# Performance work log

Measured on AMD Instinct MI355X. Metric: run time of the kernel, lower is better.

## Reference

```python
import jax, jax.numpy as jnp
import numpy as np

D = 64        # GatedGraphConv out_channels
N_LAYERS = 5  # number of stacked convs


def setup_inputs() -> dict:
    key = jax.random.key(0)
    ks = jax.random.split(key, 16)
    N, E, G = 100000, 1600000, 64
    s = 0.1
    inp = {
        'conv_weight': jax.random.normal(ks[0], (N_LAYERS, D, D), jnp.float32) * s,
        'gru_w_ih':    jax.random.normal(ks[1], (N_LAYERS, 3 * D, D), jnp.float32) * s,
        'gru_w_hh':    jax.random.normal(ks[2], (N_LAYERS, 3 * D, D), jnp.float32) * s,
        'gru_b_ih':    jax.random.normal(ks[3], (N_LAYERS, 3 * D), jnp.float32) * s,
        'gru_b_hh':    jax.random.normal(ks[4], (N_LAYERS, 3 * D), jnp.float32) * s,
        'fc1_w': jax.random.normal(ks[5], (32, D), jnp.float32) * s,
        'fc1_b': jax.random.normal(ks[6], (32,), jnp.float32) * s,
        'fc2_w': jax.random.normal(ks[7], (16, 32), jnp.float32) * s,
        'fc2_b': jax.random.normal(ks[8], (16,), jnp.float32) * s,
        'fc3_w': jax.random.normal(ks[9], (1, 16), jnp.float32) * s,
        'fc3_b': jax.random.normal(ks[10], (1,), jnp.float32) * s,
        'edge_index': jax.random.randint(ks[11], (2, E), 0, N, jnp.int64 if jax.config.jax_enable_x64 else jnp.int32),
        'batch': jnp.sort(jax.random.randint(ks[12], (N,), 0, G, jnp.int32)),
        'num_nodes': N,
        'num_graphs': G,
    }
    return inp


def _gru_cell(m, h, w_ih, w_hh, b_ih, b_hh):
    # torch.nn.GRUCell math; m: [N,D] input, h: [N,D] hidden
    gi = m @ w_ih.T + b_ih   # [N, 3D]
    gh = h @ w_hh.T + b_hh   # [N, 3D]
    i_r, i_z, i_n = jnp.split(gi, 3, axis=1)
    h_r, h_z, h_n = jnp.split(gh, 3, axis=1)
    r = jax.nn.sigmoid(i_r + h_r)
    z = jax.nn.sigmoid(i_z + h_z)
    n = jnp.tanh(i_n + r * h_n)
    return (1.0 - z) * n + z * h


def reference(conv_weight, gru_w_ih, gru_w_hh, gru_b_ih, gru_b_hh,
              fc1_w, fc1_b, fc2_w, fc2_b, fc3_w, fc3_b,
              edge_index, batch, num_nodes, num_graphs):
    src, dst = edge_index[0], edge_index[1]  # source_to_target flow
    # initial node features: zeros [N,8] zero-padded to D by GatedGraphConv
    x0 = jnp.zeros((num_nodes, D), jnp.float32)

    def step(x, params):
        w, wih, whh, bih, bhh = params
        m = x @ w                                        # [N, D]
        agg = jax.ops.segment_sum(m[src], dst, num_segments=num_nodes)  # scatter-add
        return _gru_cell(agg, x, wih, whh, bih, bhh), None

    x, _ = jax.lax.scan(step, x0,
                        (conv_weight, gru_w_ih, gru_w_hh, gru_b_ih, gru_b_hh))

    # scatter_add pooling over batch -> [num_graphs, D]
    g = jax.ops.segment_sum(x, batch, num_segments=num_graphs)
    h = jax.nn.elu(g @ fc1_w.T + fc1_b)
    h = jax.nn.elu(h @ fc2_w.T + fc2_b)
    return h @ fc3_w.T + fc3_b  # [num_graphs, 1]
```

## Files before the change

### kernel.cpp

```cpp
#include <hip/hip_runtime.h>
#include <math.h>

typedef _Float16 f16x2 __attribute__((ext_vector_type(2)));
typedef _Float16 f16x4 __attribute__((ext_vector_type(4)));
typedef _Float16 f16x8 __attribute__((ext_vector_type(8)));
typedef float f32x4 __attribute__((ext_vector_type(4)));

#define CBITS 10
#define FCHUNK 4096
#define MATSZ 13056
__device__ __forceinline__ int woff(int row) { return 64 * row + 8 * (row >> 1); }

__device__ __forceinline__ float sigmoidf_(float v) {
  return 1.0f / (1.0f + __expf(-v));
}
__device__ __forceinline__ float tanhf_(float v) {
  v = fminf(fmaxf(v, -15.f), 15.f);
  float e = __expf(2.f * v);
  return (e - 1.f) / (e + 1.f);
}
__device__ __forceinline__ float eluf_(float v) { return v > 0.f ? v : (__expf(v) - 1.f); }

__global__ __launch_bounds__(256) void fuse_w_kernel(const float* __restrict__ conv_w,
                                                     const float* __restrict__ w_ih,
                                                     _Float16* __restrict__ wcS) {
  const int l = blockIdx.x >> 2;
  const int j0 = (blockIdx.x & 3) * 48;
  const float* W = conv_w + (size_t)l * 4096;
  const float* wi = w_ih + (size_t)l * 12288;
  _Float16* out = wcS + (size_t)l * MATSZ;
  __shared__ float sWt[64 * 68];
  __shared__ float sI[48 * 64];
  const int t = threadIdx.x;
  for (int i = t; i < 4096; i += 256) sWt[(i & 63) * 68 + (i >> 6)] = W[i];
  for (int i = t; i < 3072; i += 256) sI[i] = wi[j0 * 64 + i];
  __syncthreads();
#pragma unroll
  for (int r = 0; r < 3; ++r) {
    int u = t + 256 * r;
    int j = u >> 4, cg = (u & 15) * 4;
    float4 a = {0.f, 0.f, 0.f, 0.f};
    for (int k = 0; k < 64; ++k) {
      float4 w = *(const float4*)(sWt + k * 68 + cg);
      float s = sI[j * 64 + k];
      a.x += w.x * s; a.y += w.y * s; a.z += w.z * s; a.w += w.w * s;
    }
    int row = j0 + j;
    f16x4 hv;
    hv[0] = (_Float16)a.x; hv[1] = (_Float16)a.y;
    hv[2] = (_Float16)a.z; hv[3] = (_Float16)a.w;
    *(f16x4*)(out + woff(row) + cg) = hv;
  }
}

__global__ __launch_bounds__(256) void whh_prep_kernel(const float* __restrict__ whh,
                                                       _Float16* __restrict__ whhS) {
  int idx = blockIdx.x * 256 + threadIdx.x;
  if (idx >= 15360) return;
  int l = idx / 3072, rem = idx % 3072;
  int r = rem >> 4, c4 = (rem & 15) * 4;
  float4 v = *(const float4*)(whh + (size_t)l * 12288 + r * 64 + c4);
  f16x4 hv;
  hv[0] = (_Float16)v.x; hv[1] = (_Float16)v.y;
  hv[2] = (_Float16)v.z; hv[3] = (_Float16)v.w;
  *(f16x4*)(whhS + (size_t)l * MATSZ + woff(r) + c4) = hv;
}

__global__ __launch_bounds__(256) void bucket_hist_kernel(const int* __restrict__ dst,
                                                          int* __restrict__ bh, int E) {
  __shared__ int h[128];
  const int t = threadIdx.x;
  if (t < 128) h[t] = 0;
  __syncthreads();
  for (int e = blockIdx.x * 256 + t; e < E; e += gridDim.x * 256)
    atomicAdd(&h[dst[e] >> CBITS], 1);
  __syncthreads();
  if (t < 128 && h[t]) atomicAdd(&bh[t * 16], h[t]);
}

__global__ __launch_bounds__(128) void bucket_scan_kernel(int* __restrict__ bh, int nbk,
                                                          int* __restrict__ boffs, int E) {
  __shared__ int s[128];
  const int t = threadIdx.x;
  int v = (t < nbk) ? bh[t * 16] : 0;
  s[t] = v;
  __syncthreads();
  for (int o = 1; o < 128; o <<= 1) {
    int a = (t >= o) ? s[t - o] : 0;
    __syncthreads();
    s[t] += a;
    __syncthreads();
  }
  if (t < nbk) {
    int ex = s[t] - v;
    boffs[t] = ex;
    bh[t * 16] = ex;
  }
  if (t == 0) boffs[nbk] = E;
}

__global__ __launch_bounds__(256) void bucket_fill_kernel(const int* __restrict__ src,
                                                          const int* __restrict__ dst,
                                                          int* __restrict__ bcur,
                                                          unsigned* __restrict__ pairs, int E) {
  __shared__ uint2 staged[FCHUNK];
  __shared__ int h[128], lbase[128], gbase[128], lcur[128];
  const int t = threadIdx.x;
  const int e0 = blockIdx.x * FCHUNK;
  int cnt = E - e0;
  if (cnt > FCHUNK) cnt = FCHUNK;
  if (t < 128) h[t] = 0;
  __syncthreads();
  for (int i = t; i < cnt; i += 256) atomicAdd(&h[dst[e0 + i] >> CBITS], 1);
  __syncthreads();
  if (t < 128) lcur[t] = h[t];
  __syncthreads();
  for (int o = 1; o < 128; o <<= 1) {
    int a = 0;
    if (t < 128 && t >= o) a = lcur[t - o];
    __syncthreads();
    if (t < 128) lcur[t] += a;
    __syncthreads();
  }
  if (t < 128) {
    int ex = lcur[t] - h[t];
    lbase[t] = ex;
    if (h[t]) gbase[t] = atomicAdd(&bcur[t * 16], h[t]);
    lcur[t] = ex;
  }
  __syncthreads();
  for (int i = t; i < cnt; i += 256) {
    int d = dst[e0 + i];
    int b = d >> CBITS;
    int p = atomicAdd(&lcur[b], 1);
    staged[p] = make_uint2((unsigned)src[e0 + i], (unsigned)d);
  }
  __syncthreads();
  for (int i = t; i < cnt; i += 256) {
    uint2 pr = staged[i];
    int b = (int)(pr.y >> CBITS);
    pairs[gbase[b] + (i - lbase[b])] = (pr.x << CBITS) | (pr.y & ((1u << CBITS) - 1));
  }
}

__global__ __launch_bounds__(256) void csr_build_kernel(const unsigned* __restrict__ pairs,
                                                        const int* __restrict__ boffs,
                                                        int* __restrict__ offs,
                                                        int* __restrict__ srcs, int N, int E) {
  const int b = blockIdx.x, t = threadIdx.x;
  const int nbase = b << CBITS;
  __shared__ int deg[1024];
  __shared__ int ssc[256];
  for (int i = t; i < 1024; i += 256) deg[i] = 0;
  __syncthreads();
  const int beg = boffs[b], end = boffs[b + 1];
  for (int e = beg + t; e < end; e += 256) atomicAdd(&deg[pairs[e] & 1023], 1);
  __syncthreads();
  int d0 = deg[4 * t], d1 = deg[4 * t + 1], d2 = deg[4 * t + 2], d3 = deg[4 * t + 3];
  int s = d0 + d1 + d2 + d3;
  ssc[t] = s;
  __syncthreads();
  for (int o = 1; o < 256; o <<= 1) {
    int a = (t >= o) ? ssc[t - o] : 0;
    __syncthreads();
    ssc[t] += a;
    __syncthreads();
  }
  int base = beg + ssc[t] - s;
  int c0 = base, c1 = c0 + d0, c2 = c1 + d1, c3 = c2 + d2;
  if (nbase + 4 * t + 0 < N) offs[nbase + 4 * t + 0] = c0;
  if (nbase + 4 * t + 1 < N) offs[nbase + 4 * t + 1] = c1;
  if (nbase + 4 * t + 2 < N) offs[nbase + 4 * t + 2] = c2;
  if (nbase + 4 * t + 3 < N) offs[nbase + 4 * t + 3] = c3;
  deg[4 * t] = c0; deg[4 * t + 1] = c1; deg[4 * t + 2] = c2; deg[4 * t + 3] = c3;
  if (b == 0 && t == 0) offs[N] = E;
  if (b == 0 && t < 64) srcs[E + t] = 0;
  __syncthreads();
  for (int e = beg + t; e < end; e += 256) {
    unsigned p = pairs[e];
    int pos = atomicAdd(&deg[p & 1023], 1);
    srcs[pos] = (int)(p >> CBITS);
  }
}

__global__ __launch_bounds__(64) void h1_kernel(const float* __restrict__ b_ih,
                                                const float* __restrict__ b_hh,
                                                float* __restrict__ h1) {
  int d = threadIdx.x;
  float r = sigmoidf_(b_ih[d] + b_hh[d]);
  float z = sigmoidf_(b_ih[64 + d] + b_hh[64 + d]);
  float n = tanhf_(b_ih[128 + d] + r * b_hh[128 + d]);
  h1[d] = (1.f - z) * n;
}

__global__ __launch_bounds__(256) void l1u_kernel(const _Float16* __restrict__ wcS1,
                                                  const _Float16* __restrict__ whhS1,
                                                  const float* __restrict__ h1,
                                                  const float* __restrict__ b_ih1,
                                                  const float* __restrict__ b_hh1,
                                                  float* __restrict__ u,
                                                  float* __restrict__ cons) {
  int j = threadIdx.x;
  if (j >= 192) return;
  float su = 0.f, sg = 0.f;
  const int base = woff(j);
  for (int c = 0; c < 64; ++c) {
    float hc = h1[c];
    su += hc * (float)wcS1[base + c];
    sg += hc * (float)whhS1[base + c];
  }
  u[j] = su;
  if (j < 128) {
    cons[j] = sg + b_ih1[j] + b_hh1[j];
  } else {
    cons[j] = b_ih1[j];
    cons[j + 64] = sg + b_hh1[j];
  }
}

__global__ __launch_bounds__(256) void l1_elem_kernel(const int* __restrict__ offs,
                                                      const float* __restrict__ h1,
                                                      const float* __restrict__ u,
                                                      const float* __restrict__ cons,
                                                      _Float16* __restrict__ xh,
                                                      int N, int units) {
  int idx = blockIdx.x * 256 + threadIdx.x;
  if (idx >= units) return;
  int v = idx >> 5, lp = idx & 31;
  float dg = (v < N) ? (float)(offs[v + 1] - offs[v]) : 0.f;
  f16x2 o;
#pragma unroll
  for (int k = 0; k < 2; ++k) {
    int d = 2 * lp + k;
    float r = sigmoidf_(dg * u[d] + cons[d]);
    float z = sigmoidf_(dg * u[64 + d] + cons[64 + d]);
    float n = tanhf_(dg * u[128 + d] + cons[128 + d] + r * cons[192 + d]);
    o[k] = (_Float16)(n + z * (h1[d] - n));
  }
  *(f16x2*)(xh + (size_t)idx * 2) = o;
}

__global__ __launch_bounds__(256) void agg_kernel(const _Float16* __restrict__ xh,
                                                  const int* __restrict__ offs,
                                                  const int* __restrict__ srcs,
                                                  _Float16* __restrict__ aggh, int N) {
  int wave = threadIdx.x >> 6, lane = threadIdx.x & 63;
  int v = blockIdx.x * 4 + wave;
  if (v >= N) return;
  const int beg = offs[v], end = offs[v + 1];
  const int deg = end - beg;
  const int og = lane >> 3;
  const int lp = lane & 7;
  f16x8 acc = {};
  for (int base = 0; base < deg; base += 64) {
    const int cnt = min(64, deg - base);
    int sidx = srcs[beg + base + lane];
    for (int e = 0; e < cnt; e += 8) {
      int me = e + og;
      int s = __shfl(sidx, me);
      f16x8 vv = *(const f16x8*)(xh + (size_t)s * 64 + lp * 8);
      if (me < cnt) acc += vv;
    }
  }
#pragma unroll
  for (int off = 8; off < 64; off <<= 1) {
    union { f16x8 h; int i[4]; } a, b;
    a.h = acc;
#pragma unroll
    for (int w = 0; w < 4; ++w) b.i[w] = __shfl_xor(a.i[w], off);
    acc += b.h;
  }
  if (og == 0) *(f16x8*)(aggh + (size_t)v * 64 + lp * 8) = acc;
}

__global__ __launch_bounds__(256) void gru_kernel(const _Float16* __restrict__ aggh,
                                                  const _Float16* __restrict__ xh_in,
                                                  _Float16* __restrict__ xh_out,
                                                  const _Float16* __restrict__ wcS,
                                                  const _Float16* __restrict__ whhS,
                                                  const float* __restrict__ b_ih,
                                                  const float* __restrict__ b_hh,
                                                  int N, int numIter) {
  __shared__ _Float16 sW[2 * MATSZ];
  const int t = threadIdx.x;
  for (int i = t; i < 2 * (MATSZ / 8); i += 256) {
    int mat = (i >= MATSZ / 8);
    int idx = i - mat * (MATSZ / 8);
    *(f16x8*)(sW + mat * MATSZ + idx * 8) =
        *(const f16x8*)((mat ? whhS : wcS) + idx * 8);
  }
  __syncthreads();
  const int wave = t >> 6, lane = t & 63;
  const int q = lane >> 4, c = lane & 15;
  float bRZ[4], bZZ[4], bIN[4], bHN[4];
#pragma unroll
  for (int dt = 0; dt < 4; ++dt) {
    int d = dt * 16 + c;
    bRZ[dt] = b_ih[d] + b_hh[d];
    bZZ[dt] = b_ih[64 + d] + b_hh[64 + d];
    bIN[dt] = b_ih[128 + d];
    bHN[dt] = b_hh[128 + d];
  }
  f16x8 idf[2];
#pragma unroll
  for (int p = 0; p < 2; ++p) {
    int tgt = p * 16 + c - q * 8;
#pragma unroll
    for (int j = 0; j < 8; ++j) idf[p][j] = (j == tgt) ? (_Float16)1.0f : (_Float16)0.0f;
  }
#pragma unroll 1
  for (int it = blockIdx.x; it < numIter; it += gridDim.x) {
    const int tile = it >> 1, half = it & 1;
    const int nb0 = tile * 64 + wave * 16;
    const size_t rowbase = (size_t)(nb0 + c) * 64;
    f16x8 aA[2], aH[2];
#pragma unroll
    for (int ks = 0; ks < 2; ++ks) {
      aA[ks] = *(const f16x8*)(aggh + rowbase + ks * 32 + q * 8);
      aH[ks] = *(const f16x8*)(xh_in + rowbase + ks * 32 + q * 8);
    }
    f32x4 aR[2], aZ[2], aN[2], aHNa[2], aHO[2];
#pragma unroll
    for (int p = 0; p < 2; ++p) {
      float brz = half ? bRZ[2 + p] : bRZ[p];
      float bzz = half ? bZZ[2 + p] : bZZ[p];
      float bin = half ? bIN[2 + p] : bIN[p];
      float bhn = half ? bHN[2 + p] : bHN[p];
      aR[p] = (f32x4){brz, brz, brz, brz};
      aZ[p] = (f32x4){bzz, bzz, bzz, bzz};
      aN[p] = (f32x4){bin, bin, bin, bin};
      aHNa[p] = (f32x4){bhn, bhn, bhn, bhn};
      aHO[p] = (f32x4){0.f, 0.f, 0.f, 0.f};
    }
#pragma unroll
    for (int ks = 0; ks < 2; ++ks) {
      const int colo = ks * 32 + q * 8;
#pragma unroll
      for (int p = 0; p < 2; ++p) {
        const int r0 = (half * 2 + p) * 16 + c;
        f16x8 bWr = *(const f16x8*)(sW + woff(r0) + colo);
        f16x8 bHr = *(const f16x8*)(sW + MATSZ + woff(r0) + colo);
        f16x8 bWz = *(const f16x8*)(sW + woff(64 + r0) + colo);
        f16x8 bHz = *(const f16x8*)(sW + MATSZ + woff(64 + r0) + colo);
        f16x8 bWn = *(const f16x8*)(sW + woff(128 + r0) + colo);
        f16x8 bHn = *(const f16x8*)(sW + MATSZ + woff(128 + r0) + colo);
        aR[p] = __builtin_amdgcn_mfma_f32_16x16x32_f16(aA[ks], bWr, aR[p], 0, 0, 0);
        aR[p] = __builtin_amdgcn_mfma_f32_16x16x32_f16(aH[ks], bHr, aR[p], 0, 0, 0);
        aZ[p] = __builtin_amdgcn_mfma_f32_16x16x32_f16(aA[ks], bWz, aZ[p], 0, 0, 0);
        aZ[p] = __builtin_amdgcn_mfma_f32_16x16x32_f16(aH[ks], bHz, aZ[p], 0, 0, 0);
        aN[p] = __builtin_amdgcn_mfma_f32_16x16x32_f16(aA[ks], bWn, aN[p], 0, 0, 0);
        aHNa[p] = __builtin_amdgcn_mfma_f32_16x16x32_f16(aH[ks], bHn, aHNa[p], 0, 0, 0);
      }
    }
#pragma unroll
    for (int p = 0; p < 2; ++p)
      aHO[p] = __builtin_amdgcn_mfma_f32_16x16x32_f16(aH[half], idf[p], aHO[p], 0, 0, 0);
#pragma unroll
    for (int p = 0; p < 2; ++p) {
      int d = (half * 2 + p) * 16 + c;
#pragma unroll
      for (int r = 0; r < 4; ++r) {
        int node = nb0 + q * 4 + r;
        if (node < N) {
          float rr = sigmoidf_(aR[p][r]);
          float zz = sigmoidf_(aZ[p][r]);
          float nn = tanhf_(aN[p][r] + rr * aHNa[p][r]);
          float out = nn + zz * (aHO[p][r] - nn);
          xh_out[(size_t)node * 64 + d] = (_Float16)out;
        }
      }
    }
  }
}

__global__ __launch_bounds__(256) void pool_kernel(const _Float16* __restrict__ xh,
                                                   const int* __restrict__ batch,
                                                   float* __restrict__ g, int N) {
  int wave = threadIdx.x >> 6, lane = threadIdx.x & 63;
  int n0 = blockIdx.x * 64 + wave * 16;
  if (n0 >= N) return;
  int end = n0 + 16;
  if (end > N) end = N;
  int cur = batch[n0];
  float acc = 0.f;
  for (int n = n0; n < end; ++n) {
    int b = batch[n];
    if (b != cur) {
      atomicAdd(&g[(size_t)cur * 64 + lane], acc);
      acc = 0.f;
      cur = b;
    }
    acc += (float)xh[(size_t)n * 64 + lane];
  }
  atomicAdd(&g[(size_t)cur * 64 + lane], acc);
}

__global__ __launch_bounds__(256) void mlp_kernel(const float* __restrict__ g,
                                                  const float* __restrict__ w1,
                                                  const float* __restrict__ b1,
                                                  const float* __restrict__ w2,
                                                  const float* __restrict__ b2,
                                                  const float* __restrict__ w3,
                                                  const float* __restrict__ b3,
                                                  float* __restrict__ out, int G) {
  __shared__ float sG[64 * 64];
  __shared__ float sH1[64 * 32];
  __shared__ float sH2[64 * 16];
  int t = threadIdx.x;
  for (int i = t; i < G * 64; i += 256) sG[i] = g[i];
  __syncthreads();
  for (int o = t; o < G * 32; o += 256) {
    int gi = o >> 5, i = o & 31;
    float a = b1[i];
    for (int k = 0; k < 64; ++k) a += sG[gi * 64 + k] * w1[i * 64 + k];
    sH1[gi * 32 + i] = eluf_(a);
  }
  __syncthreads();
  for (int o = t; o < G * 16; o += 256) {
    int gi = o >> 4, i = o & 15;
    float a = b2[i];
    for (int k = 0; k < 32; ++k) a += sH1[gi * 32 + k] * w2[i * 32 + k];
    sH2[gi * 16 + i] = eluf_(a);
  }
  __syncthreads();
  for (int o = t; o < G; o += 256) {
    float a = b3[0];
    for (int k = 0; k < 16; ++k) a += sH2[o * 16 + k] * w3[k];
    out[o] = a;
  }
}

extern "C" void kernel_launch(void* const* d_in, const int* in_sizes, int n_in,
                              void* d_out, int out_size, void* d_ws, size_t ws_size,
                              hipStream_t stream) {
  const float* conv_w = (const float*)d_in[0];
  const float* w_ih = (const float*)d_in[1];
  const float* w_hh = (const float*)d_in[2];
  const float* b_ih = (const float*)d_in[3];
  const float* b_hh = (const float*)d_in[4];
  const float* fc1_w = (const float*)d_in[5];
  const float* fc1_b = (const float*)d_in[6];
  const float* fc2_w = (const float*)d_in[7];
  const float* fc2_b = (const float*)d_in[8];
  const float* fc3_w = (const float*)d_in[9];
  const float* fc3_b = (const float*)d_in[10];
  const int* ei = (const int*)d_in[11];
  const int* batch = (const int*)d_in[12];
  const int N = in_sizes[12];
  const int E = in_sizes[11] / 2;
  const int G = out_size;
  const int* src = ei;
  const int* dst = ei + E;
  const int nbk = (N + 1023) >> CBITS;
  const int tiles = (N + 63) / 64;
  const int Npad = tiles * 64;
  const int gruIter = tiles * 2;

  char* ws = (char*)d_ws;
  size_t off = 0;
  auto alloc = [&](size_t bytes) -> void* {
    void* p = ws + off;
    off += (bytes + 255) & ~(size_t)255;
    return p;
  };
  _Float16* xhA = (_Float16*)alloc((size_t)Npad * 64 * 2);
  _Float16* xhB = (_Float16*)alloc((size_t)Npad * 64 * 2);
  _Float16* aggh = (_Float16*)alloc((size_t)Npad * 64 * 2);
  _Float16* wcS = (_Float16*)alloc((size_t)5 * MATSZ * 2);
  _Float16* whhS = (_Float16*)alloc((size_t)5 * MATSZ * 2);
  float* h1 = (float*)alloc(64 * 4);
  float* l1u = (float*)alloc(192 * 4);
  float* l1c = (float*)alloc(256 * 4);
  float* gbuf = (float*)alloc((size_t)G * 64 * 4);
  int* offs = (int*)alloc((size_t)(N + 1) * 4);
  int* srcs = (int*)alloc((size_t)(E + 64) * 4);
  unsigned* pairs = (unsigned*)alloc((size_t)E * 4);
  int* bh = (int*)alloc(128 * 16 * 4);
  int* boffs = (int*)alloc(129 * 4);

  hipMemsetAsync(bh, 0, 128 * 16 * 4, stream);
  bucket_hist_kernel<<<256, 256, 0, stream>>>(dst, bh, E);
  bucket_scan_kernel<<<1, 128, 0, stream>>>(bh, nbk, boffs, E);
  bucket_fill_kernel<<<(E + FCHUNK - 1) / FCHUNK, 256, 0, stream>>>(src, dst, bh, pairs, E);
  csr_build_kernel<<<nbk, 256, 0, stream>>>(pairs, boffs, offs, srcs, N, E);

  fuse_w_kernel<<<20, 256, 0, stream>>>(conv_w, w_ih, wcS);
  whh_prep_kernel<<<60, 256, 0, stream>>>(w_hh, whhS);

  h1_kernel<<<1, 64, 0, stream>>>(b_ih, b_hh, h1);
  l1u_kernel<<<1, 256, 0, stream>>>(wcS + MATSZ, whhS + MATSZ, h1,
                                    b_ih + 192, b_hh + 192, l1u, l1c);
  l1_elem_kernel<<<(Npad * 32 + 255) / 256, 256, 0, stream>>>(offs, h1, l1u, l1c, xhA,
                                                              N, Npad * 32);

  _Float16* cur = xhA;
  _Float16* nxt = xhB;
  for (int l = 2; l < 5; ++l) {
    agg_kernel<<<(N + 3) / 4, 256, 0, stream>>>(cur, offs, srcs, aggh, N);
    gru_kernel<<<768, 256, 0, stream>>>(aggh, cur, nxt, wcS + (size_t)l * MATSZ,
                                        whhS + (size_t)l * MATSZ, b_ih + (size_t)l * 192,
                                        b_hh + (size_t)l * 192, N, gruIter);
    _Float16* tmp = cur; cur = nxt; nxt = tmp;
  }

  hipMemsetAsync(gbuf, 0, (size_t)G * 64 * 4, stream);
  pool_kernel<<<(N + 63) / 64, 256, 0, stream>>>(cur, batch, gbuf, N);
  mlp_kernel<<<1, 256, 0, stream>>>(gbuf, fc1_w, fc1_b, fc2_w, fc2_b, fc3_w, fc3_b,
                                    (float*)d_out, G);
}
```

Baseline: 409.5 us.

## Drop GRU shared-memory weight staging, merge tiny prep kernels, fold memset

The GRU kernel no longer copies both weight matrices into LDS per block and instead reads B-fragments straight from global memory (through the caches), and it is now launched with gruIter blocks instead of a fixed 768. The h1 and layer-1 prep kernels are merged into one launch, and the pooling buffer memset is folded into the bucket scan kernel. This removes the per-block LDS fill and barrier plus two launches, but the repeated global weight loads inside the MFMA loop depend on L1/L2 hits and could add latency.

```diff
diff --git a/kernel.cpp b/kernel.cpp
--- a/kernel.cpp
+++ b/kernel.cpp
@@ -79,9 +79,11 @@
 }
 
 __global__ __launch_bounds__(128) void bucket_scan_kernel(int* __restrict__ bh, int nbk,
-                                                          int* __restrict__ boffs, int E) {
+                                                          int* __restrict__ boffs, int E,
+                                                          float* __restrict__ gbuf, int gn) {
   __shared__ int s[128];
   const int t = threadIdx.x;
+  for (int i = t; i < gn; i += 128) gbuf[i] = 0.f;
   int v = (t < nbk) ? bh[t * 16] : 0;
   s[t] = v;
   __syncthreads();
@@ -183,29 +185,31 @@
   }
 }
 
-__global__ __launch_bounds__(64) void h1_kernel(const float* __restrict__ b_ih,
-                                                const float* __restrict__ b_hh,
-                                                float* __restrict__ h1) {
-  int d = threadIdx.x;
-  float r = sigmoidf_(b_ih[d] + b_hh[d]);
-  float z = sigmoidf_(b_ih[64 + d] + b_hh[64 + d]);
-  float n = tanhf_(b_ih[128 + d] + r * b_hh[128 + d]);
-  h1[d] = (1.f - z) * n;
-}
-
-__global__ __launch_bounds__(256) void l1u_kernel(const _Float16* __restrict__ wcS1,
-                                                  const _Float16* __restrict__ whhS1,
-                                                  const float* __restrict__ h1,
-                                                  const float* __restrict__ b_ih1,
-                                                  const float* __restrict__ b_hh1,
-                                                  float* __restrict__ u,
-                                                  float* __restrict__ cons) {
+__global__ __launch_bounds__(256) void l01_prep_kernel(const float* __restrict__ b_ih0,
+                                                       const float* __restrict__ b_hh0,
+                                                       const _Float16* __restrict__ wcS1,
+                                                       const _Float16* __restrict__ whhS1,
+                                                       const float* __restrict__ b_ih1,
+                                                       const float* __restrict__ b_hh1,
+                                                       float* __restrict__ h1,
+                                                       float* __restrict__ u,
+                                                       float* __restrict__ cons) {
+  __shared__ float sh1[64];
   int j = threadIdx.x;
+  if (j < 64) {
+    float r = sigmoidf_(b_ih0[j] + b_hh0[j]);
+    float z = sigmoidf_(b_ih0[64 + j] + b_hh0[64 + j]);
+    float n = tanhf_(b_ih0[128 + j] + r * b_hh0[128 + j]);
+    float h = (1.f - z) * n;
+    sh1[j] = h;
+    h1[j] = h;
+  }
+  __syncthreads();
   if (j >= 192) return;
   float su = 0.f, sg = 0.f;
   const int base = woff(j);
   for (int c = 0; c < 64; ++c) {
-    float hc = h1[c];
+    float hc = sh1[c];
     su += hc * (float)wcS1[base + c];
     sg += hc * (float)whhS1[base + c];
   }
@@ -281,15 +285,7 @@
                                                   const float* __restrict__ b_ih,
                                                   const float* __restrict__ b_hh,
                                                   int N, int numIter) {
-  __shared__ _Float16 sW[2 * MATSZ];
   const int t = threadIdx.x;
-  for (int i = t; i < 2 * (MATSZ / 8); i += 256) {
-    int mat = (i >= MATSZ / 8);
-    int idx = i - mat * (MATSZ / 8);
-    *(f16x8*)(sW + mat * MATSZ + idx * 8) =
-        *(const f16x8*)((mat ? whhS : wcS) + idx * 8);
-  }
-  __syncthreads();
   const int wave = t >> 6, lane = t & 63;
   const int q = lane >> 4, c = lane & 15;
   float bRZ[4], bZZ[4], bIN[4], bHN[4];
@@ -338,12 +334,12 @@
 #pragma unroll
       for (int p = 0; p < 2; ++p) {
         const int r0 = (half * 2 + p) * 16 + c;
-        f16x8 bWr = *(const f16x8*)(sW + woff(r0) + colo);
-        f16x8 bHr = *(const f16x8*)(sW + MATSZ + woff(r0) + colo);
-        f16x8 bWz = *(const f16x8*)(sW + woff(64 + r0) + colo);
-        f16x8 bHz = *(const f16x8*)(sW + MATSZ + woff(64 + r0) + colo);
-        f16x8 bWn = *(const f16x8*)(sW + woff(128 + r0) + colo);
-        f16x8 bHn = *(const f16x8*)(sW + MATSZ + woff(128 + r0) + colo);
+        f16x8 bWr = *(const f16x8*)(wcS + woff(r0) + colo);
+        f16x8 bHr = *(const f16x8*)(whhS + woff(r0) + colo);
+        f16x8 bWz = *(const f16x8*)(wcS + woff(64 + r0) + colo);
+        f16x8 bHz = *(const f16x8*)(whhS + woff(64 + r0) + colo);
+        f16x8 bWn = *(const f16x8*)(wcS + woff(128 + r0) + colo);
+        f16x8 bHn = *(const f16x8*)(whhS + woff(128 + r0) + colo);
         aR[p] = __builtin_amdgcn_mfma_f32_16x16x32_f16(aA[ks], bWr, aR[p], 0, 0, 0);
         aR[p] = __builtin_amdgcn_mfma_f32_16x16x32_f16(aH[ks], bHr, aR[p], 0, 0, 0);
         aZ[p] = __builtin_amdgcn_mfma_f32_16x16x32_f16(aA[ks], bWz, aZ[p], 0, 0, 0);
@@ -480,16 +476,15 @@
 
   hipMemsetAsync(bh, 0, 128 * 16 * 4, stream);
   bucket_hist_kernel<<<256, 256, 0, stream>>>(dst, bh, E);
-  bucket_scan_kernel<<<1, 128, 0, stream>>>(bh, nbk, boffs, E);
+  bucket_scan_kernel<<<1, 128, 0, stream>>>(bh, nbk, boffs, E, gbuf, G * 64);
   bucket_fill_kernel<<<(E + FCHUNK - 1) / FCHUNK, 256, 0, stream>>>(src, dst, bh, pairs, E);
   csr_build_kernel<<<nbk, 256, 0, stream>>>(pairs, boffs, offs, srcs, N, E);
 
   fuse_w_kernel<<<20, 256, 0, stream>>>(conv_w, w_ih, wcS);
   whh_prep_kernel<<<60, 256, 0, stream>>>(w_hh, whhS);
 
-  h1_kernel<<<1, 64, 0, stream>>>(b_ih, b_hh, h1);
-  l1u_kernel<<<1, 256, 0, stream>>>(wcS + MATSZ, whhS + MATSZ, h1,
-                                    b_ih + 192, b_hh + 192, l1u, l1c);
+  l01_prep_kernel<<<1, 256, 0, stream>>>(b_ih, b_hh, wcS + MATSZ, whhS + MATSZ,
+                                         b_ih + 192, b_hh + 192, h1, l1u, l1c);
   l1_elem_kernel<<<(Npad * 32 + 255) / 256, 256, 0, stream>>>(offs, h1, l1u, l1c, xhA,
                                                               N, Npad * 32);
 
@@ -497,13 +492,12 @@
   _Float16* nxt = xhB;
   for (int l = 2; l < 5; ++l) {
     agg_kernel<<<(N + 3) / 4, 256, 0, stream>>>(cur, offs, srcs, aggh, N);
-    gru_kernel<<<768, 256, 0, stream>>>(aggh, cur, nxt, wcS + (size_t)l * MATSZ,
-                                        whhS + (size_t)l * MATSZ, b_ih + (size_t)l * 192,
-                                        b_hh + (size_t)l * 192, N, gruIter);
+    gru_kernel<<<gruIter, 256, 0, stream>>>(aggh, cur, nxt, wcS + (size_t)l * MATSZ,
+                                            whhS + (size_t)l * MATSZ, b_ih + (size_t)l * 192,
+                                            b_hh + (size_t)l * 192, N, gruIter);
     _Float16* tmp = cur; cur = nxt; nxt = tmp;
   }
 
-  hipMemsetAsync(gbuf, 0, (size_t)G * 64 * 4, stream);
   pool_kernel<<<(N + 63) / 64, 256, 0, stream>>>(cur, batch, gbuf, N);
   mlp_kernel<<<1, 256, 0, stream>>>(gbuf, fc1_w, fc1_b, fc2_w, fc2_b, fc3_w, fc3_b,
                                     (float*)d_out, G);
```

Measured after the change: 469.6 us. 1.15x slower.
